# Kernel optimization log

Hardware: AMD Instinct MI355X
Metric: run time of the kernel (lower is better)

The kernel has to match this reference:

```python
import jax, jax.numpy as jnp
import numpy as np

NUM_BINS = 512  # 8 levels per RGB channel: (R>>5)<<6 + (G>>5)<<3 + (B>>5)


def _color_histograms(frames):
    # frames: [B, T, H, W, 3] int32, values in [0, 256)
    B, T, H, W, _ = frames.shape
    f = frames.reshape(B * T, H * W, 3)
    R, G, Bc = f[:, :, 0], f[:, :, 1], f[:, :, 2]
    binned = ((R >> 5) << 6) + ((G >> 5) << 3) + (Bc >> 5)  # [BT, HW] in [0,512)
    prefix = (jnp.arange(B * T, dtype=jnp.int32) << 9)[:, None]  # frame offset (512 bins/frame)
    idx = (binned + prefix).reshape(-1)
    hist = jnp.zeros(B * T * NUM_BINS, dtype=jnp.int32).at[idx].add(jnp.int32(1))
    hist = hist.reshape(B, T, NUM_BINS).astype(jnp.float32)
    # F.normalize(p=2, dim=2, eps=1e-12)
    norm = jnp.sqrt(jnp.sum(hist * hist, axis=2, keepdims=True))
    return hist / jnp.maximum(norm, 1e-12)


def setup_inputs() -> dict:
    key = jax.random.key(0)
    k1, k2, k3 = jax.random.split(key, 3)
    frames = jax.random.randint(k1, (16, 256, 64, 64, 3), 0, 256, dtype=jnp.int32)
    fc_w = jax.random.normal(k2, (128, 101), dtype=jnp.float32) * 0.1
    fc_b = jax.random.normal(k3, (128,), dtype=jnp.float32) * 0.01
    return {"frames": frames, "fc_w": fc_w, "fc_b": fc_b}


def reference(frames, fc_w, fc_b):
    lookup_window = fc_w.shape[1]
    half = (lookup_window - 1) // 2
    x = _color_histograms(frames)  # [B, T, 512]
    B, T, _ = x.shape
    sim = jnp.einsum('btd,bsd->bts', x, x)  # [B, T, T]
    sim_padded = jnp.pad(sim, ((0, 0), (0, 0), (half, half)))  # [B, T, T+W-1]
    t_idx = jnp.arange(T)[:, None]                    # [T, 1]
    l_idx = t_idx + jnp.arange(lookup_window)[None, :]  # [T, W]
    windowed = sim_padded[:, t_idx, l_idx]            # [B, T, W]
    return jax.nn.relu(jnp.einsum('btw,ow->bto', windowed, fc_w) + fc_b)
```

## Files before the change

kernel.cpp:

```cpp
#include <hip/hip_runtime.h>
#include <hip/hip_bf16.h>

#define NUM_BINS 512
#define T_LEN 256
#define B_LEN 16
#define WIN 101
#define HALF 50
#define NOUT 128

typedef __attribute__((ext_vector_type(8))) short short8;
typedef __attribute__((ext_vector_type(4))) float f32x4;

__device__ __forceinline__ unsigned short f2bf(float f) {
    unsigned u = __float_as_uint(f);
    u += 0x7fff + ((u >> 16) & 1);
    return (unsigned short)(u >> 16);
}

__global__ __launch_bounds__(256, 6) void hist_kernel(const int* __restrict__ frames,
                                                      const float* __restrict__ fc_w,
                                                      __hip_bfloat16* __restrict__ xout,
                                                      unsigned short* __restrict__ fcswz) {
    const int tid = threadIdx.x;
    const int bid = blockIdx.x;

    if (bid >= 2048) {
        const int base = (bid - 2048) * 2048 + tid * 8;
        const int l15 = (base >> 3) & 15;
        const int kg = (base >> 7) & 3;
        const int ks = (base >> 9) & 3;
        const int og = base >> 11;
        const int o = og * 16 + l15;
        short8 v;
        #pragma unroll
        for (int e = 0; e < 8; ++e) {
            const int w = ks * 32 + kg * 8 + e;
            v[e] = (short)((w < WIN) ? f2bf(fc_w[o * WIN + w]) : (unsigned short)0);
        }
        *(short8*)(fcswz + base) = v;
        return;
    }

    __shared__ int hist[2][NUM_BINS];
    __shared__ float red[2][4];

    hist[0][tid] = 0; hist[0][tid + 256] = 0;
    hist[1][tid] = 0; hist[1][tid + 256] = 0;
    __syncthreads();

    const int4* f4 = (const int4*)(frames + (size_t)bid * 24576);

    #pragma unroll
    for (int i = 0; i < 4; ++i) {
        const int q = (i * 256 + tid) * 3;
        int4 a = f4[q + 0];
        int4 b = f4[q + 1];
        int4 c = f4[q + 2];
        atomicAdd(&hist[0][((a.x >> 5) << 6) | ((a.y >> 5) << 3) | (a.z >> 5)], 1);
        atomicAdd(&hist[0][((a.w >> 5) << 6) | ((b.x >> 5) << 3) | (b.y >> 5)], 1);
        atomicAdd(&hist[0][((b.z >> 5) << 6) | ((b.w >> 5) << 3) | (c.x >> 5)], 1);
        atomicAdd(&hist[0][((c.y >> 5) << 6) | ((c.z >> 5) << 3) | (c.w >> 5)], 1);
    }
    __syncthreads();

    #pragma unroll
    for (int i = 0; i < 4; ++i) {
        const int q = 3072 + (i * 256 + tid) * 3;
        int4 a = f4[q + 0];
        int4 b = f4[q + 1];
        int4 c = f4[q + 2];
        atomicAdd(&hist[1][((a.x >> 5) << 6) | ((a.y >> 5) << 3) | (a.z >> 5)], 1);
        atomicAdd(&hist[1][((a.w >> 5) << 6) | ((b.x >> 5) << 3) | (b.y >> 5)], 1);
        atomicAdd(&hist[1][((b.z >> 5) << 6) | ((b.w >> 5) << 3) | (c.x >> 5)], 1);
        atomicAdd(&hist[1][((c.y >> 5) << 6) | ((c.z >> 5) << 3) | (c.w >> 5)], 1);
    }

    const int lane = tid & 63;
    const int wave = tid >> 6;

    const int a0 = hist[0][tid];
    const int a1 = hist[0][tid + 256];
    float ss0 = (float)a0 * (float)a0 + (float)a1 * (float)a1;
    #pragma unroll
    for (int off = 32; off; off >>= 1) ss0 += __shfl_down(ss0, off, 64);
    if (lane == 0) red[0][wave] = ss0;
    __syncthreads();
    {
        const float inv = 1.0f / sqrtf(red[0][0] + red[0][1] + red[0][2] + red[0][3]);
        __hip_bfloat16* xrow = xout + (size_t)(bid * 2) * NUM_BINS;
        xrow[tid] = __float2bfloat16((float)a0 * inv);
        xrow[tid + 256] = __float2bfloat16((float)a1 * inv);
    }
    const int b0 = hist[1][tid];
    const int b1 = hist[1][tid + 256];
    float ss1 = (float)b0 * (float)b0 + (float)b1 * (float)b1;
    #pragma unroll
    for (int off = 32; off; off >>= 1) ss1 += __shfl_down(ss1, off, 64);
    if (lane == 0) red[1][wave] = ss1;
    __syncthreads();
    {
        const float inv = 1.0f / sqrtf(red[1][0] + red[1][1] + red[1][2] + red[1][3]);
        __hip_bfloat16* xrow = xout + (size_t)(bid * 2 + 1) * NUM_BINS;
        xrow[tid] = __float2bfloat16((float)b0 * inv);
        xrow[tid + 256] = __float2bfloat16((float)b1 * inv);
    }
}

__global__ __launch_bounds__(512) void simfc_kernel(const unsigned short* __restrict__ x,
                                                    const unsigned short* __restrict__ fcswz,
                                                    const float* __restrict__ fc_b,
                                                    float* __restrict__ out) {
    __shared__ float sim_lds[16 * 132];
    __shared__ unsigned short win_lds[16 * 136];

    const int bid = blockIdx.x;
    const int b = bid & 15;
    const int tt = bid >> 4;
    const int t0 = tt * 16;
    const int tid = threadIdx.x;
    const int lane = tid & 63;
    const int wave = tid >> 6;
    const int l15 = lane & 15;
    const int kg = lane >> 4;

    const unsigned short* xb = x + (size_t)b * T_LEN * NUM_BINS;

    {
        f32x4 acc = {0.f, 0.f, 0.f, 0.f};
        const short8 zero8 = {0, 0, 0, 0, 0, 0, 0, 0};
        const int rowA = t0 + l15;
        const int rb = t0 - HALF + 16 * wave + l15;
        const bool vv = (rb >= 0) && (rb < T_LEN);
        const int rc = min(max(rb, 0), T_LEN - 1);
        const unsigned short* pa = xb + (size_t)rowA * NUM_BINS + kg * 8;
        const unsigned short* ps = xb + (size_t)rc * NUM_BINS + kg * 8;
        #pragma unroll
        for (int ks = 0; ks < 16; ++ks) {
            short8 a  = *(const short8*)(pa + ks * 32);
            short8 bb = *(const short8*)(ps + ks * 32);
            bb = vv ? bb : zero8;
            acc = __builtin_amdgcn_mfma_f32_16x16x32_bf16(a, bb, acc, 0, 0, 0);
        }
        #pragma unroll
        for (int r = 0; r < 4; ++r)
            sim_lds[(kg * 4 + r) * 132 + wave * 16 + l15] = acc[r];
    }
    __syncthreads();

    if (tid < 256) {
        const int i = tid >> 4;
        const int w8 = (tid & 15) * 8;
        short8 v;
        #pragma unroll
        for (int e = 0; e < 8; ++e) {
            const int w = w8 + e;
            const float fv = (w < WIN) ? sim_lds[i * 132 + i + w] : 0.0f;
            v[e] = (short)f2bf(fv);
        }
        *(short8*)(&win_lds[i * 136 + w8]) = v;
    }
    __syncthreads();

    {
        f32x4 o0 = {0.f, 0.f, 0.f, 0.f};
        const int o = wave * 16 + l15;
        #pragma unroll
        for (int ks = 0; ks < 4; ++ks) {
            short8 a = *(const short8*)(&win_lds[l15 * 136 + ks * 32 + kg * 8]);
            short8 b0 = *(const short8*)(fcswz + ((((wave * 4 + ks) * 4 + kg) * 16 + l15) * 8));
            o0 = __builtin_amdgcn_mfma_f32_16x16x32_bf16(a, b0, o0, 0, 0, 0);
        }
        const float bias = fc_b[o];
        float* ob = out + ((size_t)b * T_LEN + t0) * NOUT;
        #pragma unroll
        for (int r = 0; r < 4; ++r)
            ob[(kg * 4 + r) * NOUT + o] = fmaxf(o0[r] + bias, 0.0f);
    }
}

extern "C" void kernel_launch(void* const* d_in, const int* in_sizes, int n_in,
                              void* d_out, int out_size, void* d_ws, size_t ws_size,
                              hipStream_t stream) {
    const int* frames = (const int*)d_in[0];
    const float* fc_w = (const float*)d_in[1];
    const float* fc_b = (const float*)d_in[2];
    float* out = (float*)d_out;
    __hip_bfloat16* x = (__hip_bfloat16*)d_ws;
    unsigned short* fcswz = (unsigned short*)((char*)d_ws + (4 << 20));

    hist_kernel<<<2048 + 8, 256, 0, stream>>>(frames, fc_w, x, fcswz);
    simfc_kernel<<<256, 512, 0, stream>>>((const unsigned short*)x, fcswz, fc_b, out);
}
```

Measured before the change: 44.03 us.

## Use one-wave blocks per frame with parity-split LDS histogram

```diff
diff --git a/kernel.cpp b/kernel.cpp
--- a/kernel.cpp
+++ b/kernel.cpp
@@ -17,15 +17,15 @@
     return (unsigned short)(u >> 16);
 }
 
-__global__ __launch_bounds__(256, 6) void hist_kernel(const int* __restrict__ frames,
-                                                      const float* __restrict__ fc_w,
-                                                      __hip_bfloat16* __restrict__ xout,
-                                                      unsigned short* __restrict__ fcswz) {
-    const int tid = threadIdx.x;
+__global__ __launch_bounds__(64) void hist_kernel(const int* __restrict__ frames,
+                                                  const float* __restrict__ fc_w,
+                                                  __hip_bfloat16* __restrict__ xout,
+                                                  unsigned short* __restrict__ fcswz) {
     const int bid = blockIdx.x;
+    const int lane = threadIdx.x;
 
-    if (bid >= 2048) {
-        const int base = (bid - 2048) * 2048 + tid * 8;
+    if (bid >= 4096) {
+        const int base = (bid - 4096) * 512 + lane * 8;
         const int l15 = (base >> 3) & 15;
         const int kg = (base >> 7) & 3;
         const int ks = (base >> 9) & 3;
@@ -41,69 +41,51 @@
         return;
     }
 
-    __shared__ int hist[2][NUM_BINS];
-    __shared__ float red[2][4];
+    __shared__ int hist[2 * NUM_BINS];
 
-    hist[0][tid] = 0; hist[0][tid + 256] = 0;
-    hist[1][tid] = 0; hist[1][tid + 256] = 0;
+    {
+        const int4 z = {0, 0, 0, 0};
+        #pragma unroll
+        for (int i = 0; i < 4; ++i)
+            *(int4*)(&hist[i * 256 + lane * 4]) = z;
+    }
     __syncthreads();
 
-    const int4* f4 = (const int4*)(frames + (size_t)bid * 24576);
-
-    #pragma unroll
-    for (int i = 0; i < 4; ++i) {
-        const int q = (i * 256 + tid) * 3;
+    const int par = lane & 1;
+    const int4* f4 = (const int4*)(frames + (size_t)bid * 12288);
+    #pragma unroll 4
+    for (int i = 0; i < 16; ++i) {
+        const int q = (i * 64 + lane) * 3;
         int4 a = f4[q + 0];
         int4 b = f4[q + 1];
         int4 c = f4[q + 2];
-        atomicAdd(&hist[0][((a.x >> 5) << 6) | ((a.y >> 5) << 3) | (a.z >> 5)], 1);
-        atomicAdd(&hist[0][((a.w >> 5) << 6) | ((b.x >> 5) << 3) | (b.y >> 5)], 1);
-        atomicAdd(&hist[0][((b.z >> 5) << 6) | ((b.w >> 5) << 3) | (c.x >> 5)], 1);
-        atomicAdd(&hist[0][((c.y >> 5) << 6) | ((c.z >> 5) << 3) | (c.w >> 5)], 1);
+        atomicAdd(&hist[(((a.x >> 5) << 7) | ((a.y >> 5) << 4) | ((a.z >> 5) << 1)) | par], 1);
+        atomicAdd(&hist[(((a.w >> 5) << 7) | ((b.x >> 5) << 4) | ((b.y >> 5) << 1)) | par], 1);
+        atomicAdd(&hist[(((b.z >> 5) << 7) | ((b.w >> 5) << 4) | ((c.x >> 5) << 1)) | par], 1);
+        atomicAdd(&hist[(((c.y >> 5) << 7) | ((c.z >> 5) << 4) | ((c.w >> 5) << 1)) | par], 1);
     }
     __syncthreads();
 
+    int h[8];
+    {
+        const int4* hp = (const int4*)(&hist[lane * 16]);
+        int4 a = hp[0], b = hp[1], c = hp[2], d = hp[3];
+        h[0] = a.x + a.y; h[1] = a.z + a.w;
+        h[2] = b.x + b.y; h[3] = b.z + b.w;
+        h[4] = c.x + c.y; h[5] = c.z + c.w;
+        h[6] = d.x + d.y; h[7] = d.z + d.w;
+    }
+    float ss = 0.0f;
     #pragma unroll
-    for (int i = 0; i < 4; ++i) {
-        const int q = 3072 + (i * 256 + tid) * 3;
-        int4 a = f4[q + 0];
-        int4 b = f4[q + 1];
-        int4 c = f4[q + 2];
-        atomicAdd(&hist[1][((a.x >> 5) << 6) | ((a.y >> 5) << 3) | (a.z >> 5)], 1);
-        atomicAdd(&hist[1][((a.w >> 5) << 6) | ((b.x >> 5) << 3) | (b.y >> 5)], 1);
-        atomicAdd(&hist[1][((b.z >> 5) << 6) | ((b.w >> 5) << 3) | (c.x >> 5)], 1);
-        atomicAdd(&hist[1][((c.y >> 5) << 6) | ((c.z >> 5) << 3) | (c.w >> 5)], 1);
-    }
+    for (int j = 0; j < 8; ++j) ss += (float)h[j] * (float)h[j];
+    #pragma unroll
+    for (int off = 1; off < 64; off <<= 1) ss += __shfl_xor(ss, off, 64);
+    const float inv = 1.0f / sqrtf(ss);
 
-    const int lane = tid & 63;
-    const int wave = tid >> 6;
-
-    const int a0 = hist[0][tid];
-    const int a1 = hist[0][tid + 256];
-    float ss0 = (float)a0 * (float)a0 + (float)a1 * (float)a1;
+    short8 v;
     #pragma unroll
-    for (int off = 32; off; off >>= 1) ss0 += __shfl_down(ss0, off, 64);
-    if (lane == 0) red[0][wave] = ss0;
-    __syncthreads();
-    {
-        const float inv = 1.0f / sqrtf(red[0][0] + red[0][1] + red[0][2] + red[0][3]);
-        __hip_bfloat16* xrow = xout + (size_t)(bid * 2) * NUM_BINS;
-        xrow[tid] = __float2bfloat16((float)a0 * inv);
-        xrow[tid + 256] = __float2bfloat16((float)a1 * inv);
-    }
-    const int b0 = hist[1][tid];
-    const int b1 = hist[1][tid + 256];
-    float ss1 = (float)b0 * (float)b0 + (float)b1 * (float)b1;
-    #pragma unroll
-    for (int off = 32; off; off >>= 1) ss1 += __shfl_down(ss1, off, 64);
-    if (lane == 0) red[1][wave] = ss1;
-    __syncthreads();
-    {
-        const float inv = 1.0f / sqrtf(red[1][0] + red[1][1] + red[1][2] + red[1][3]);
-        __hip_bfloat16* xrow = xout + (size_t)(bid * 2 + 1) * NUM_BINS;
-        xrow[tid] = __float2bfloat16((float)b0 * inv);
-        xrow[tid + 256] = __float2bfloat16((float)b1 * inv);
-    }
+    for (int j = 0; j < 8; ++j) v[j] = (short)f2bf((float)h[j] * inv);
+    *(short8*)((unsigned short*)xout + (size_t)bid * NUM_BINS + lane * 8) = v;
 }
 
 __global__ __launch_bounds__(512) void simfc_kernel(const unsigned short* __restrict__ x,
@@ -188,6 +170,6 @@
     __hip_bfloat16* x = (__hip_bfloat16*)d_ws;
     unsigned short* fcswz = (unsigned short*)((char*)d_ws + (4 << 20));
 
-    hist_kernel<<<2048 + 8, 256, 0, stream>>>(frames, fc_w, x, fcswz);
+    hist_kernel<<<4096 + 32, 64, 0, stream>>>(frames, fc_w, x, fcswz);
     simfc_kernel<<<256, 512, 0, stream>>>((const unsigned short*)x, fcswz, fc_b, out);
 }
```

After: 43.78 us, median of 2. Within noise of the previous version (-0.6%).
